# Optimization experiments

Hardware: AMD Instinct MI355X
Metric: run time of the kernel (lower is better)

The kernel has to match this reference:

```python
import jax, jax.numpy as jnp
import numpy as np

B, E, F, Q = 16, 2048, 8192, 20
D, WD = 256, 300
NUM_ENTITY, NUM_WORD, NUM_RELATION = 100000, 50000, 600
NUM_LAYER = 3
PAGERANK_LAMBDA = 0.8
FACT_SCALE = 3.0
VERY_NEG = -100000000000.0
VERY_SMALL = 1e-10


def setup_inputs() -> dict:
    key = jax.random.key(0)
    ks = jax.random.split(key, 40)
    s = 0.05
    L = NUM_LAYER
    inp = {
        'local_entity': jax.random.randint(ks[0], (B, E), 0, NUM_ENTITY),
        'q2e_adj_mat': jax.random.uniform(ks[1], (B, E, 1), jnp.float32),
        'kb_fact_rel': jax.random.randint(ks[2], (B, F), 0, NUM_RELATION),
        'query_text': jax.random.randint(ks[3], (B, Q), 0, NUM_WORD),
        'answer_dist': jax.random.uniform(ks[4], (B, E), jnp.float32),
        'e2f_ent': jax.random.randint(ks[5], (B, F), 0, E),
        'f2e_ent': jax.random.randint(ks[6], (B, F), 0, E),
        'word_emb': jax.random.normal(ks[7], (NUM_WORD + 1, WD)) * s,
        'entity_emb': jax.random.normal(ks[8], (NUM_ENTITY + 1, WD)) * s,
        'relation_emb': jax.random.normal(ks[9], (NUM_RELATION + 1, 2 * WD)) * s,
        'entity_lin_w': jax.random.normal(ks[10], (D, WD)) * s,
        'entity_lin_b': jnp.zeros((D,)),
        'relation_lin_w': jax.random.normal(ks[11], (D, 2 * WD)) * s,
        'relation_lin_b': jnp.zeros((D,)),
        'lstm_w_ih': jax.random.normal(ks[12], (4 * D, WD)) * s,
        'lstm_w_hh': jax.random.normal(ks[13], (4 * D, D)) * s,
        'lstm_b_ih': jnp.zeros((4 * D,)),
        'lstm_b_hh': jnp.zeros((4 * D,)),
        'q2e_w': jax.random.normal(ks[14], (L, D, D)) * s,
        'q2e_b': jnp.zeros((L, D)),
        'e2q_w': jax.random.normal(ks[15], (L, D, 3 * D)) * s,
        'e2q_b': jnp.zeros((L, D)),
        'e2e_w': jax.random.normal(ks[16], (L, D, 3 * D)) * s,
        'e2e_b': jnp.zeros((L, D)),
        'kb_head_w': jax.random.normal(ks[17], (L, D, D)) * s,
        'kb_head_b': jnp.zeros((L, D)),
        'kb_tail_w': jax.random.normal(ks[18], (L, D, D)) * s,
        'kb_tail_b': jnp.zeros((L, D)),
        'kb_self_w': jax.random.normal(ks[19], (L, D, D)) * s,
        'kb_self_b': jnp.zeros((L, D)),
        'score_w': jax.random.normal(ks[20], (1, D)) * s,
        'score_b': jnp.zeros((1,)),
    }
    return inp


def _lstm(x, w_ih, w_hh, b_ih, b_hh):
    # torch LSTM, single layer, unidirectional, zero init state; gates (i,f,g,o)
    gx = jnp.einsum('btd,gd->btg', x, w_ih) + b_ih + b_hh  # [B,T,4H]
    H = w_hh.shape[1]
    init = (jnp.zeros((x.shape[0], H), x.dtype), jnp.zeros((x.shape[0], H), x.dtype))
    def step(carry, g):
        h, c = carry
        z = g + h @ w_hh.T
        i, f, gg, o = jnp.split(z, 4, axis=-1)
        c = jax.nn.sigmoid(f) * c + jax.nn.sigmoid(i) * jnp.tanh(gg)
        h = jax.nn.sigmoid(o) * jnp.tanh(c)
        return (h, c), h
    (h, _), hs = jax.lax.scan(step, init, jnp.swapaxes(gx, 0, 1))
    return jnp.swapaxes(hs, 0, 1), h  # [B,T,H], [B,H]


def _forward(local_entity, q2e_adj_mat, kb_fact_rel, query_text, e2f_ent, f2e_ent,
             word_emb, entity_emb, relation_emb,
             entity_lin_w, entity_lin_b, relation_lin_w, relation_lin_b,
             lstm_w_ih, lstm_w_hh, lstm_b_ih, lstm_b_hh,
             q2e_w, q2e_b, e2q_w, e2q_b, e2e_w, e2e_b,
             kb_head_w, kb_head_b, kb_tail_w, kb_tail_b, kb_self_w, kb_self_b,
             score_w, score_b):
    bidx = jnp.arange(B)[:, None]
    ent_mask = (local_entity != NUM_ENTITY).astype(jnp.float32)  # [B,E]
    q_mask = (query_text != NUM_WORD).astype(jnp.float32)        # [B,Q]

    # query LSTM encoding (dropout = identity in eval)
    qh, qlast = _lstm(word_emb[query_text], lstm_w_ih, lstm_w_hh, lstm_b_ih, lstm_b_hh)
    query_node = qlast[:, None, :]                               # [B,1,D]

    # fact embeddings
    lf = relation_emb[kb_fact_rel] @ relation_lin_w.T + relation_lin_b  # [B,F,D]
    div = jnp.sqrt(jnp.float32(D))

    # fact <-> query attention
    sim = jnp.einsum('bqd,bfd->bqf', qh, lf) / div
    sim = jax.nn.softmax(sim + (1.0 - q_mask)[:, :, None] * VERY_NEG, axis=1)
    att = jnp.einsum('bqf,bqd->bfd', sim, qh)
    Wf = jnp.sum(att * lf, axis=2) / div                          # [B,F]
    W_tilde = jnp.exp(Wf - jnp.max(Wf, axis=1, keepdims=True))    # [B,F]

    # e2f softmax normalizer: scatter-add fact weights onto head entities
    e2f_softmax = jnp.zeros((B, E), W_tilde.dtype).at[bidx, e2f_ent].add(W_tilde)
    e2f_softmax = jnp.maximum(e2f_softmax, VERY_SMALL)

    # entity embeddings (word_dim != entity_dim -> linear projection)
    le = entity_emb[local_entity] @ entity_lin_w.T + entity_lin_b  # [B,E,D]
    pagerank = q2e_adj_mat[..., 0]                                 # [B,E]

    for i in range(NUM_LAYER):
        q2e = jnp.broadcast_to(query_node @ q2e_w[i].T + q2e_b[i], (B, E, D))
        # fact update: self + gathered head-entity messages
        fact_self = lf @ kb_self_w[i].T + kb_self_b[i]
        head = le @ kb_head_w[i].T + kb_head_b[i]
        e2f_emb = jax.nn.relu(fact_self + jnp.take_along_axis(head, e2f_ent[:, :, None], axis=1))
        norm = W_tilde * jnp.take_along_axis(pagerank / e2f_softmax, e2f_ent, axis=1)  # [B,F]
        e2f_emb = e2f_emb * norm[:, :, None]
        # entity update: self + scattered tail messages
        tail = e2f_emb @ kb_tail_w[i].T + kb_tail_b[i]
        ent_self = le @ kb_self_w[i].T + kb_self_b[i]
        f2e_emb = jax.nn.relu(ent_self + jnp.zeros((B, E, D), le.dtype).at[bidx, f2e_ent].add(tail))
        pagerank = (PAGERANK_LAMBDA * jnp.zeros((B, E), norm.dtype).at[bidx, f2e_ent].add(norm)
                    + (1.0 - PAGERANK_LAMBDA) * pagerank)
        nxt = jnp.concatenate([le, q2e, FACT_SCALE * f2e_emb], axis=2)  # [B,E,3D]
        query_node = jnp.einsum('be,bed->bd', pagerank, nxt @ e2q_w[i].T + e2q_b[i])[:, None, :]
        le = jax.nn.relu(nxt @ e2e_w[i].T + e2e_b[i])

    score = (le @ score_w.T + score_b)[..., 0]                     # [B,E]
    return score


def reference(local_entity, q2e_adj_mat, kb_fact_rel, query_text, answer_dist,
              e2f_ent, f2e_ent, word_emb, entity_emb, relation_emb,
              entity_lin_w, entity_lin_b, relation_lin_w, relation_lin_b,
              lstm_w_ih, lstm_w_hh, lstm_b_ih, lstm_b_hh,
              q2e_w, q2e_b, e2q_w, e2q_b, e2e_w, e2e_b,
              kb_head_w, kb_head_b, kb_tail_w, kb_tail_b, kb_self_w, kb_self_b,
              score_w, score_b):
    return _forward(local_entity, q2e_adj_mat, kb_fact_rel, query_text, e2f_ent, f2e_ent,
                    word_emb, entity_emb, relation_emb,
                    entity_lin_w, entity_lin_b, relation_lin_w, relation_lin_b,
                    lstm_w_ih, lstm_w_hh, lstm_b_ih, lstm_b_hh,
                    q2e_w, q2e_b, e2q_w, e2q_b, e2e_w, e2e_b,
                    kb_head_w, kb_head_b, kb_tail_w, kb_tail_b, kb_self_w, kb_self_b,
                    score_w, score_b)
```

## Files before the change

### kernel.cpp

```cpp
#include <hip/hip_runtime.h>
#include <hip/hip_bf16.h>

typedef __hip_bfloat16 bf16;
typedef __attribute__((ext_vector_type(8))) short bf16x8;
typedef __attribute__((ext_vector_type(4))) float f32x4;

#define BB 16
#define EE 2048
#define FF 8192
#define QQ 20
#define DD 256
#define WDIM 300
#define NWORD 50000
#define VERY_NEG_F (-1.0e11f)

static __device__ __forceinline__ float b2f(bf16 x){ return __bfloat162float(x); }
static __device__ __forceinline__ bf16 f2b(float x){ return __float2bfloat16(x); }
static __device__ __forceinline__ float sigm(float x){ return 1.f/(1.f+expf(-x)); }
static __device__ __forceinline__ void ld4bf(const bf16* p, float v[4]){
  short4 s = *(const short4*)p;
  v[0]=b2f(*(const bf16*)&s.x); v[1]=b2f(*(const bf16*)&s.y);
  v[2]=b2f(*(const bf16*)&s.z); v[3]=b2f(*(const bf16*)&s.w);
}
static __device__ __forceinline__ void st4bf(bf16* p, float a,float b,float c,float d){
  unsigned short u[4]; bf16 t;
  t=f2b(a);u[0]=*(unsigned short*)&t; t=f2b(b);u[1]=*(unsigned short*)&t;
  t=f2b(c);u[2]=*(unsigned short*)&t; t=f2b(d);u[3]=*(unsigned short*)&t;
  *(short4*)p=*(short4*)u;
}

#define O_GX       0UL
#define O_QH       1310720UL
#define O_QNODE    1638400UL
#define O_RELLIN   1654784UL
#define O_WR       2270208UL
#define O_WMAX     2308864UL
#define O_WT       2309120UL
#define O_E2FS     2833408UL
#define O_PR       2964480UL
#define O_PRAGG    3095552UL
#define O_Q2EV     3226624UL
#define O_Q2EVB    3243008UL
#define O_RELSELF  3251200UL
#define O_NORM     3866624UL
#define O_WNXT     4390912UL
#define O_PRSUM    4440064UL
#define O_CNT      4440320UL
#define O_CUR      4571392UL
#define O_BSTART   4702464UL
#define O_BIDX     4834048UL
#define O_ELWPAD   5358336UL
#define O_FLAG     5522176UL
#define O_CVT      5522432UL
#define O_AGG      10915584UL
#define O_ENTSELF  27692800UL
#define O_LEA      44470016UL
#define O_LEB      61247232UL
#define O_HEAD     78024448UL
#define O_F2EEMB   94801664UL

#define C_ELB   0
#define C_RLW   256
#define C_RLB   153856
#define C_WIH   154112
#define C_WHH   461312
#define C_BIH   723456
#define C_BHH   724480
#define C_Q2EW  725504
#define C_Q2EB  922112
#define C_E2QW  922880
#define C_E2QB  1512704
#define C_E2EW  1513472
#define C_E2EB  2103296
#define C_KHW   2104064
#define C_KHB   2300672
#define C_KTW   2301440
#define C_KTB   2498048
#define C_KSW   2498816
#define C_KSB   2695424
#define C_SCW   2696192
#define C_SCB   2696448

__global__ __launch_bounds__(256) void k_sniff(const unsigned short* ee, int* flag){
  __shared__ int red[256];
  int c=0;
  for(int i=threadIdx.x;i<4096;i+=256){
    int ex=(ee[2*i]>>7)&0xFF;
    c += (ex>=192);
  }
  red[threadIdx.x]=c; __syncthreads();
  for(int o=128;o;o>>=1){ if(threadIdx.x<o) red[threadIdx.x]+=red[threadIdx.x+o]; __syncthreads(); }
  if(!threadIdx.x) flag[0] = (red[0]>64) ? 1 : 0;
}

struct CvtJobs{ const void* src[20]; bf16* dst[20]; int n[20]; int sc[20]; };
__global__ __launch_bounds__(256) void k_cvt(CvtJobs J, const int* dfl){
  const int isf=*dfl;
  int j=blockIdx.y;
  int n=J.n[j];
  int i4=(blockIdx.x*256+threadIdx.x)*4;
  if(i4>=n) return;
  float m = (J.sc[j] && ((i4%768)>=512)) ? 3.f : 1.f;
  bf16* d=J.dst[j]+i4;
  if(isf){
    const float* s=(const float*)J.src[j]+i4;
    if(i4+4<=n){ float4 t=*(const float4*)s; st4bf(d,t.x*m,t.y*m,t.z*m,t.w*m); }
    else for(int r=0;i4+r<n;r++) d[r]=f2b(s[r]*m);
  } else {
    const bf16* s=(const bf16*)J.src[j]+i4;
    if(i4+4<=n){ float v[4]; ld4bf(s,v); st4bf(d,v[0]*m,v[1]*m,v[2]*m,v[3]*m); }
    else for(int r=0;i4+r<n;r++) d[r]=f2b(b2f(s[r])*m);
  }
}

__global__ __launch_bounds__(256) void k_cvtwhh(const void* src, bf16* wf, const int* dfl){
  const int isf=*dfl;
  int fid=blockIdx.x*256+threadIdx.x;
  int lane=fid&63, kt=(fid>>6)&7, gt=fid>>9;
  int l16=lane&15, q=lane>>4;
  long so=(long)(gt*16+l16)*256 + kt*32 + q*8;
  float v[8];
  if(isf){ const float* s=(const float*)src+so;
    #pragma unroll
    for(int j=0;j<8;j++) v[j]=s[j];
  } else { const bf16* s=(const bf16*)src+so; ld4bf(s,v); ld4bf(s+4,v+4); }
  bf16* d=wf+(long)fid*8;
  st4bf(d,v[0],v[1],v[2],v[3]); st4bf(d+4,v[4],v[5],v[6],v[7]);
}

__global__ __launch_bounds__(256) void k_cvtelw(const void* src, bf16* dst, const int* dfl){
  const int isf=*dfl;
  int r=blockIdx.x;
  for(int c=threadIdx.x;c<320;c+=256){
    float v=0.f;
    if(c<300) v = isf ? ((const float*)src)[r*300+c] : b2f(((const bf16*)src)[r*300+c]);
    dst[(long)r*320+c]=f2b(v);
  }
}

__global__ __launch_bounds__(256) void k_cnt(const int* f2e, int* cnt){
  int i=blockIdx.x*256+threadIdx.x;
  atomicAdd(&cnt[((i>>13)<<11)+f2e[i]], 1);
}
__global__ __launch_bounds__(1024) void k_scan(const int* cnt, int* bstart){
  __shared__ int ps[1024];
  int t=threadIdx.x;
  int loc[32]; int s=0;
  #pragma unroll
  for(int j=0;j<32;j++){ loc[j]=s; s+=cnt[t*32+j]; }
  ps[t]=s; __syncthreads();
  for(int off=1;off<1024;off<<=1){
    int v=(t>=off)?ps[t-off]:0;
    __syncthreads(); ps[t]+=v; __syncthreads();
  }
  int base=(t? ps[t-1]:0);
  #pragma unroll
  for(int j=0;j<32;j++) bstart[t*32+j]=base+loc[j];
  if(t==1023) bstart[32768]=ps[1023];
}
__global__ __launch_bounds__(256) void k_fill(const int* f2e, const int* bstart, int* cur, int* bidx){
  int i=blockIdx.x*256+threadIdx.x;
  int key=((i>>13)<<11)+f2e[i];
  int pos=bstart[key]+atomicAdd(&cur[key],1);
  bidx[pos]=i;
}

__global__ __launch_bounds__(256) void k_gx(const int* qtext, const void* wemb,
    const bf16* wih, const bf16* bih, const bf16* bhh, float* gx, const int* dfl){
  const int isf=*dfl;
  int bt=blockIdx.x;
  __shared__ float xr[WDIM];
  int w=qtext[bt];
  for(int k4=threadIdx.x*4;k4<WDIM;k4+=1024){
    if(isf){ float4 t=*(const float4*)((const float*)wemb+(long)w*WDIM+k4);
             xr[k4]=t.x;xr[k4+1]=t.y;xr[k4+2]=t.z;xr[k4+3]=t.w; }
    else   { float v[4]; ld4bf((const bf16*)wemb+(long)w*WDIM+k4,v);
             xr[k4]=v[0];xr[k4+1]=v[1];xr[k4+2]=v[2];xr[k4+3]=v[3]; }
  }
  __syncthreads();
  #pragma unroll
  for(int s=0;s<4;s++){
    int g=threadIdx.x+256*s;
    float acc=b2f(bih[g])+b2f(bhh[g]);
    const bf16* wr=wih+(long)g*WDIM;
    for(int k4=0;k4<WDIM;k4+=4){
      float v[4]; ld4bf(wr+k4,v);
      acc+=v[0]*xr[k4]+v[1]*xr[k4+1]+v[2]*xr[k4+2]+v[3]*xr[k4+3];
    }
    gx[bt*1024+g]=acc;
  }
}

#define NLB 8
__global__ __launch_bounds__(512) void k_mega(const float* gx, const bf16* wf,
    float* qh, float* qnode, bf16* hbuf, int* lcnt,
    const void* remb, const bf16* rlw, const bf16* rlb, float* rel_lin,
    const int* local_entity, const void* emb, bf16* A0,
    const void* adj, float* pr, const int* dfl){
  const int bid=blockIdx.x, tid=threadIdx.x;
  if(bid<NLB){
    __shared__ bf16  hlds[16*264];
    __shared__ float zs[4*16*32];
    __shared__ bf16  hsl[512];
    const int k=bid;
    const int wv=tid>>6, lane=tid&63, q=lane>>4, l16=lane&15;
    const int gt=(wv>>1)*16 + k*2 + (wv&1);
    const int b=tid>>5, u=tid&31, gu=k*32+u;
    bf16x8 wreg[8];
    #pragma unroll
    for(int kt=0;kt<8;kt++)
      wreg[kt]=*(const bf16x8*)(wf + (((long)(gt*8+kt))*64 + lane)*8);
    float c=0.f;
    float gxr[4];
    #pragma unroll
    for(int g=0;g<4;g++) gxr[g]=gx[(b*QQ+0)*1024 + g*256 + gu];
    for(int t=0;t<QQ;t++){
      f32x4 acc=(f32x4){0.f,0.f,0.f,0.f};
      if(t){
        while(__hip_atomic_load(lcnt+(t-1), __ATOMIC_RELAXED, __HIP_MEMORY_SCOPE_AGENT) < NLB)
          __builtin_amdgcn_s_sleep(2);
        __builtin_amdgcn_fence(__ATOMIC_ACQUIRE, "agent");
        __builtin_amdgcn_sched_barrier(0);
        const bf16* hb = hbuf + (t&1)*4096;
        {
          int r=tid>>5, cc=(tid&31)*8;
          unsigned long long v0=__hip_atomic_load((const unsigned long long*)(hb + r*256 + cc),
                         __ATOMIC_RELAXED, __HIP_MEMORY_SCOPE_AGENT);
          unsigned long long v1=__hip_atomic_load((const unsigned long long*)(hb + r*256 + cc + 4),
                         __ATOMIC_RELAXED, __HIP_MEMORY_SCOPE_AGENT);
          *(unsigned long long*)&hlds[r*264 + cc] = v0;
          *(unsigned long long*)&hlds[r*264 + cc + 4] = v1;
        }
        __syncthreads();
        #pragma unroll
        for(int kt=0;kt<8;kt++){
          bf16x8 af=*(const bf16x8*)&hlds[l16*264 + kt*32 + q*8];
          acc=__builtin_amdgcn_mfma_f32_16x16x32_bf16(af,wreg[kt],acc,0,0,0);
        }
      }
      #pragma unroll
      for(int r=0;r<4;r++) zs[(wv>>1)*512 + (q*4+r)*32 + (wv&1)*16 + l16]=acc[r];
      __syncthreads();
      float zi=zs[0*512+b*32+u]+gxr[0];
      float zf=zs[1*512+b*32+u]+gxr[1];
      float zg=zs[2*512+b*32+u]+gxr[2];
      float zo=zs[3*512+b*32+u]+gxr[3];
      { int tn=(t<QQ-1)?t+1:t;
        #pragma unroll
        for(int g=0;g<4;g++) gxr[g]=gx[(b*QQ+tn)*1024 + g*256 + gu];
      }
      c=sigm(zf)*c+sigm(zi)*tanhf(zg);
      float hv=sigm(zo)*tanhf(c);
      hsl[tid]=f2b(hv);
      __syncthreads();
      if(t<QQ-1){
        if(tid<128){
          bf16* hw=hbuf + ((t+1)&1)*4096;
          int bb=tid>>3, p=tid&7;
          unsigned long long v=*(unsigned long long*)&hsl[bb*32+p*4];
          __hip_atomic_store((unsigned long long*)(hw + bb*256 + k*32 + p*4), v,
                             __ATOMIC_RELAXED, __HIP_MEMORY_SCOPE_AGENT);
        }
        __syncthreads();
        if(tid==0)
          __hip_atomic_fetch_add(lcnt+t, 1, __ATOMIC_RELAXED, __HIP_MEMORY_SCOPE_AGENT);
      }
      __builtin_nontemporal_store(hv, &qh[(long)(b*QQ+t)*256+gu]);
      if(t==QQ-1) qnode[(b<<8)+gu]=hv;
    }
  } else if(bid<309){
    __shared__ float rr[2][2*WDIM];
    const int isf=*dfl;
    const int half=tid>>8, d=tid&255;
    const int r=(bid-8)*2+half;
    if(r<601){
      for(int k4=d*4;k4<2*WDIM;k4+=1024){
        if(isf){ float4 t4=*(const float4*)((const float*)remb+(long)r*2*WDIM+k4);
                 rr[half][k4]=t4.x;rr[half][k4+1]=t4.y;rr[half][k4+2]=t4.z;rr[half][k4+3]=t4.w; }
        else   { float v[4]; ld4bf((const bf16*)remb+(long)r*2*WDIM+k4,v);
                 rr[half][k4]=v[0];rr[half][k4+1]=v[1];rr[half][k4+2]=v[2];rr[half][k4+3]=v[3]; }
      }
    }
    __syncthreads();
    if(r<601){
      float acc=b2f(rlb[d]);
      const bf16* wr=rlw+(long)d*2*WDIM;
      for(int k4=0;k4<2*WDIM;k4+=4){
        float v[4]; ld4bf(wr+k4,v);
        acc+=v[0]*rr[half][k4]+v[1]*rr[half][k4+1]+v[2]*rr[half][k4+2]+v[3]*rr[half][k4+3];
      }
      rel_lin[r*DD+d]=acc;
    }
  } else if(bid<325){
    const int isf=*dfl;
    int i4=((bid-309)*512+tid)*4;
    if(isf){ *(float4*)(pr+i4)=*(const float4*)((const float*)adj+i4); }
    else { float v[4]; ld4bf((const bf16*)adj+i4,v);
           float4 t; t.x=v[0];t.y=v[1];t.z=v[2];t.w=v[3]; *(float4*)(pr+i4)=t; }
  } else {
    const int isf=*dfl;
    int row=(bid-325)*4+(tid>>7); int t=tid&127;
    int ent=local_entity[row];
    bf16* dst=A0+(long)row*320;
    if(t<75){
      float v[4];
      if(isf){ float4 x=*(const float4*)((const float*)emb+(long)ent*WDIM+t*4);
               v[0]=x.x;v[1]=x.y;v[2]=x.z;v[3]=x.w; }
      else ld4bf((const bf16*)emb+(long)ent*WDIM+t*4, v);
      st4bf(dst+t*4, v[0],v[1],v[2],v[3]);
    } else if(t<80){
      st4bf(dst+t*4, 0.f,0.f,0.f,0.f);
    }
  }
}

__global__ __launch_bounds__(256) void k_simwr(const float* qh, const float* rel_lin,
    const int* qtext, float* Wr){
  int b = blockIdx.x, rc = blockIdx.y;
  __shared__ float qhb[QQ*DD];
  __shared__ float qm[QQ];
  for(int i=threadIdx.x;i<QQ*DD;i+=256) qhb[i]=qh[b*QQ*DD+i];
  if(threadIdx.x<QQ) qm[threadIdx.x] = (qtext[b*QQ+threadIdx.x]!=NWORD)?0.f:VERY_NEG_F;
  __syncthreads();
  int r = rc*256+threadIdx.x;
  if(r>=601) return;
  float s[QQ];
  #pragma unroll
  for(int q=0;q<QQ;q++) s[q]=0.f;
  for(int k=0;k<DD;k++){
    float rl = rel_lin[r*DD+k];
    #pragma unroll
    for(int q=0;q<QQ;q++) s[q] += qhb[q*DD+k]*rl;
  }
  float m=-1e30f;
  #pragma unroll
  for(int q=0;q<QQ;q++){ s[q]*=0.0625f; m=fmaxf(m, s[q]+qm[q]); }
  float sum=0.f, w=0.f;
  #pragma unroll
  for(int q=0;q<QQ;q++){ float p=expf(s[q]+qm[q]-m); sum+=p; w+=p*s[q]; }
  Wr[b*601+r] = w/sum;
}

__global__ __launch_bounds__(256) void k_wmax(const float* Wr, const int* rel, float* wmax){
  int b=blockIdx.x; __shared__ float red[256];
  float m=-1e30f;
  for(int f=threadIdx.x;f<FF;f+=256) m=fmaxf(m, Wr[b*601+rel[b*FF+f]]);
  red[threadIdx.x]=m; __syncthreads();
  for(int o=128;o;o>>=1){ if(threadIdx.x<o) red[threadIdx.x]=fmaxf(red[threadIdx.x],red[threadIdx.x+o]); __syncthreads(); }
  if(!threadIdx.x) wmax[b]=red[0];
}
__global__ __launch_bounds__(256) void k_wt(const float* Wr, const int* rel,
    const float* wmax, const int* e2f, float* wt, float* e2fs){
  int i = blockIdx.x*256+threadIdx.x;
  int b = i>>13;
  float v = expf(Wr[b*601+rel[i]] - wmax[b]);
  wt[i]=v;
  atomicAdd(e2fs + (b<<11) + e2f[i], v);
}

struct MG {
  const bf16* A; const bf16* W; const bf16* bias;
  bf16* out; int K;
  const bf16* Aq2; const bf16* Af2;
  const int* cnt; const bf16* addb;
  const bf16* W2; const bf16* bias2; bf16* out2;
};
template<int CONCAT,int EPI,int TK,int DUAL>
__global__ __launch_bounds__(256) void k_mgemm(MG p){
  const int m0 = blockIdx.x*64;
  const int wave = threadIdx.x>>6, lane = threadIdx.x&63;
  const int q = lane>>4, l16 = lane&15;
  const int n0 = wave*64;
  const int bidx_ = m0>>11;
  const bf16* Wp = p.W; const bf16* biasp = p.bias; bf16* outp = p.out;
  if(DUAL && blockIdx.y){ Wp=p.W2; biasp=p.bias2; outp=p.out2; }
  f32x4 acc[4][4];
  #pragma unroll
  for(int i=0;i<4;i++)
    #pragma unroll
    for(int j=0;j<4;j++) acc[i][j]=(f32x4){0.f,0.f,0.f,0.f};
  #pragma unroll
  for(int k0=0;k0<TK;k0+=32){
    int kk=k0+q*8;
    bf16x8 af[4], bw[4];
    #pragma unroll
    for(int mi=0;mi<4;mi++){
      int row=m0+mi*16+l16;
      const bf16* ap;
      if(CONCAT){
        if(kk<256)      ap=p.A  +(long)row*256+kk;
        else if(kk<512) ap=p.Aq2+(bidx_<<8)+(kk-256);
        else            ap=p.Af2+(long)row*256+(kk-512);
      } else ap=p.A+(long)row*TK+kk;
      af[mi]=*(const bf16x8*)ap;
    }
    #pragma unroll
    for(int ni=0;ni<4;ni++)
      bw[ni]=*(const bf16x8*)(Wp+(long)(n0+ni*16+l16)*TK+kk);
    #pragma unroll
    for(int mi=0;mi<4;mi++)
      #pragma unroll
      for(int ni=0;ni<4;ni++)
        acc[mi][ni]=__builtin_amdgcn_mfma_f32_16x16x32_bf16(af[mi],bw[ni],acc[mi][ni],0,0,0);
  }
  #pragma unroll
  for(int ni=0;ni<4;ni++){
    int col=n0+ni*16+l16;
    float bv=b2f(biasp[col]);
    #pragma unroll
    for(int mi=0;mi<4;mi++){
      #pragma unroll
      for(int r=0;r<4;r++){
        int row=m0+mi*16+q*4+r;
        float v=acc[mi][ni][r];
        if(EPI==0) v+=bv;
        else if(EPI==1) v=fmaxf(v+bv,0.f);
        else {
          v += (float)p.cnt[row]*bv + b2f(p.addb[(long)row*256+col]);
          v=fmaxf(v,0.f);
        }
        outp[(long)row*256+col]=f2b(v);
      }
    }
  }
}

__global__ __launch_bounds__(256) void k_small(const float* rel_lin, const bf16* selfw,
    const bf16* selfb, const float* qnode, const bf16* q2ew, const bf16* q2eb,
    float* relself, float* q2ev, bf16* q2evb){
  __shared__ float xr[DD];
  int d=threadIdx.x;
  if(blockIdx.x<601){
    int r=blockIdx.x;
    xr[d]=rel_lin[r*DD+d]; __syncthreads();
    float acc=b2f(selfb[d]);
    const bf16* wr=selfw+(long)d*DD;
    for(int k4=0;k4<DD;k4+=4){
      float v[4]; ld4bf(wr+k4,v);
      acc+=v[0]*xr[k4]+v[1]*xr[k4+1]+v[2]*xr[k4+2]+v[3]*xr[k4+3];
    }
    relself[r*DD+d]=acc;
  } else {
    int b=blockIdx.x-601;
    xr[d]=qnode[(b<<8)+d]; __syncthreads();
    float acc=b2f(q2eb[d]);
    const bf16* wr=q2ew+(long)d*DD;
    for(int k4=0;k4<DD;k4+=4){
      float v[4]; ld4bf(wr+k4,v);
      acc+=v[0]*xr[k4]+v[1]*xr[k4+1]+v[2]*xr[k4+2]+v[3]*xr[k4+3];
    }
    q2ev[(b<<8)+d]=acc;
    q2evb[(b<<8)+d]=f2b(acc);
  }
}

__global__ __launch_bounds__(256) void k_norm(const float* wt, const float* pr,
    const float* e2fs, const int* e2f, const int* f2e, float* normv, float* pragg){
  int i=blockIdx.x*256+threadIdx.x;
  int b=i>>13;
  int e=e2f[i];
  float v=wt[i]*pr[(b<<11)+e]/fmaxf(e2fs[(b<<11)+e],1e-10f);
  normv[i]=v;
  atomicAdd(pragg+(b<<11)+f2e[i], v);
}

__global__ __launch_bounds__(256) void k_agg(const int* bstart, const int* bidx,
    const int* rel, const int* e2f, const float* normv, const float* relself,
    const bf16* head, bf16* agg){
  int eidx=blockIdx.x*4+(threadIdx.x>>6);
  int lane=threadIdx.x&63;
  int b=eidx>>11;
  float a0=0.f,a1=0.f,a2=0.f,a3=0.f;
  int s=bstart[eidx], e=bstart[eidx+1];
  for(int i=s;i<e;i++){
    int f=bidx[i];
    int r=rel[f]; int ent=e2f[f]; float nv=normv[f];
    float4 rs=*(const float4*)&relself[r*DD+lane*4];
    float hd[4]; ld4bf(head+(long)(((b<<11)+ent)*DD+lane*4),hd);
    a0+=fmaxf(rs.x+hd[0],0.f)*nv; a1+=fmaxf(rs.y+hd[1],0.f)*nv;
    a2+=fmaxf(rs.z+hd[2],0.f)*nv; a3+=fmaxf(rs.w+hd[3],0.f)*nv;
  }
  st4bf(agg+(long)eidx*DD+lane*4, a0,a1,a2,a3);
}

__global__ __launch_bounds__(256) void k_wnxt(const float* pragg, float* pr, const bf16* le,
    const bf16* f2e, float* wnxt, float* prsum){
  __shared__ float r1[4*256];
  __shared__ float r3[4*256];
  __shared__ float rp[4];
  const int b=blockIdx.x, ch=blockIdx.y;
  const int wv=threadIdx.x>>6, lane=threadIdx.x&63;
  const int pe0=(b<<11)+ch*64+wv*16;
  float pv=0.f;
  if(lane<16){
    pv=0.8f*pragg[pe0+lane]+0.2f*pr[pe0+lane];
    pr[pe0+lane]=pv;
  }
  float a1[4]={0.f,0.f,0.f,0.f}, a3[4]={0.f,0.f,0.f,0.f}, ap=0.f;
  #pragma unroll
  for(int r=0;r<16;r++){
    float p=__shfl(pv, r, 64);
    long base=((long)(pe0+r))<<8;
    float v1[4],v3[4];
    ld4bf(le +base+lane*4, v1);
    ld4bf(f2e+base+lane*4, v3);
    #pragma unroll
    for(int j=0;j<4;j++){ a1[j]+=p*v1[j]; a3[j]+=p*v3[j]; }
    ap+=p;
  }
  #pragma unroll
  for(int j=0;j<4;j++){ r1[wv*256+lane*4+j]=a1[j]; r3[wv*256+lane*4+j]=a3[j]; }
  if(!lane) rp[wv]=ap;
  __syncthreads();
  const int t=threadIdx.x;
  float s1=r1[t]+r1[256+t]+r1[512+t]+r1[768+t];
  float s3=r3[t]+r3[256+t]+r3[512+t]+r3[768+t];
  atomicAdd(&wnxt[b*768+t], s1);
  atomicAdd(&wnxt[b*768+512+t], s3);
  if(!t) atomicAdd(&prsum[b], rp[0]+rp[1]+rp[2]+rp[3]);
}

__global__ __launch_bounds__(256) void k_qnode(const float* wnxt, const float* prsum,
    const float* q2ev, const bf16* w, const bf16* bias, float* qnode){
  int b=blockIdx.x, d=threadIdx.x;
  __shared__ float xr[768];
  float ps=prsum[b];
  xr[d]=wnxt[b*768+d];
  xr[256+d]=ps*q2ev[(b<<8)+d];
  xr[512+d]=wnxt[b*768+512+d];
  __syncthreads();
  float acc=0.f;
  const bf16* wr=w+(long)d*768;
  for(int k4=0;k4<768;k4+=4){
    float v[4]; ld4bf(wr+k4,v);
    acc+=v[0]*xr[k4]+v[1]*xr[k4+1]+v[2]*xr[k4+2]+v[3]*xr[k4+3];
  }
  qnode[(b<<8)+d]=acc+ps*b2f(bias[d]);
}

__global__ __launch_bounds__(256) void k_score(const bf16* le, const bf16* sw,
    const bf16* sb, void* out, const int* dfl){
  const int isf=*dfl;
  int o=blockIdx.x*4 + (threadIdx.x>>6);
  int lane=threadIdx.x&63;
  float v[4],wv[4];
  ld4bf(le+(long)o*DD+lane*4,v); ld4bf(sw+lane*4,wv);
  float acc=v[0]*wv[0]+v[1]*wv[1]+v[2]*wv[2]+v[3]*wv[3];
  for(int off=32;off;off>>=1) acc+=__shfl_down(acc,off,64);
  if(!lane){
    float r=acc+b2f(sb[0]);
    if(isf) ((float*)out)[o]=r; else ((bf16*)out)[o]=f2b(r);
  }
}

extern "C" void kernel_launch(void* const* d_in, const int* in_sizes, int n_in,
                              void* d_out, int out_size, void* d_ws, size_t ws_size,
                              hipStream_t stream){
  const int*  local_entity=(const int*)d_in[0];
  const void* q2e_adj     =d_in[1];
  const int*  kb_fact_rel =(const int*)d_in[2];
  const int*  query_text  =(const int*)d_in[3];
  const int*  e2f_ent     =(const int*)d_in[5];
  const int*  f2e_ent     =(const int*)d_in[6];
  const void* word_emb    =d_in[7];
  const void* entity_emb  =d_in[8];
  const void* relation_emb=d_in[9];

  char* ws=(char*)d_ws;
  float* gx      =(float*)(ws+O_GX);
  float* qh      =(float*)(ws+O_QH);
  float* qnode   =(float*)(ws+O_QNODE);
  float* rel_lin =(float*)(ws+O_RELLIN);
  float* Wr      =(float*)(ws+O_WR);
  float* wmax    =(float*)(ws+O_WMAX);
  float* wt      =(float*)(ws+O_WT);
  float* e2fs    =(float*)(ws+O_E2FS);
  float* pr      =(float*)(ws+O_PR);
  float* pragg   =(float*)(ws+O_PRAGG);
  float* q2ev    =(float*)(ws+O_Q2EV);
  bf16*  q2evb   =(bf16*)(ws+O_Q2EVB);
  float* relself =(float*)(ws+O_RELSELF);
  float* normv   =(float*)(ws+O_NORM);
  float* wnxt    =(float*)(ws+O_WNXT);
  float* prsum   =(float*)(ws+O_PRSUM);
  int*   cnt     =(int*)(ws+O_CNT);
  int*   cur     =(int*)(ws+O_CUR);
  int*   bstart  =(int*)(ws+O_BSTART);
  int*   bidx    =(int*)(ws+O_BIDX);
  bf16*  elwpad  =(bf16*)(ws+O_ELWPAD);
  int*   dflag   =(int*)(ws+O_FLAG);
  bf16*  cw      =(bf16*)(ws+O_CVT);
  bf16*  agg     =(bf16*)(ws+O_AGG);
  bf16*  A0      =(bf16*)(ws+O_AGG);
  bf16*  entself =(bf16*)(ws+O_ENTSELF);
  bf16*  leA     =(bf16*)(ws+O_LEA);
  bf16*  leB     =(bf16*)(ws+O_LEB);
  bf16*  headb   =(bf16*)(ws+O_HEAD);
  bf16*  f2eemb  =(bf16*)(ws+O_F2EEMB);
  bf16*  hbuf    =(bf16*)(ws+O_LEA);
  int*   lcnt    =(int*)(ws+O_LEA+16384);

  k_sniff<<<1,256,0,stream>>>((const unsigned short*)entity_emb, dflag);

  CvtJobs J;
  int cntj=0;
  auto add=[&](int in_idx, long coff, int n, int sc){
    J.src[cntj]=d_in[in_idx]; J.dst[cntj]=cw+coff; J.n[cntj]=n; J.sc[cntj]=sc; cntj++;
  };
  add(11,C_ELB,256,0);
  add(12,C_RLW,153600,0);  add(13,C_RLB,256,0);
  add(14,C_WIH,307200,0);
  add(16,C_BIH,1024,0);    add(17,C_BHH,1024,0);
  add(18,C_Q2EW,196608,0); add(19,C_Q2EB,768,0);
  add(20,C_E2QW,589824,1); add(21,C_E2QB,768,0);
  add(22,C_E2EW,589824,1); add(23,C_E2EB,768,0);
  add(24,C_KHW,196608,0);  add(25,C_KHB,768,0);
  add(26,C_KTW,196608,0);  add(27,C_KTB,768,0);
  add(28,C_KSW,196608,0);  add(29,C_KSB,768,0);
  add(30,C_SCW,256,0);     add(31,C_SCB,1,0);
  k_cvt<<<dim3(576,20),256,0,stream>>>(J, dflag);
  k_cvtwhh<<<128,256,0,stream>>>(d_in[15], cw+C_WHH, dflag);
  k_cvtelw<<<256,256,0,stream>>>(d_in[10], elwpad, dflag);

  hipMemsetAsync(cnt, 0, (size_t)2*BB*EE*4, stream);
  k_cnt <<<BB*FF/256,256,0,stream>>>(f2e_ent, cnt);
  k_scan<<<1,1024,0,stream>>>(cnt, bstart);
  k_fill<<<BB*FF/256,256,0,stream>>>(f2e_ent, bstart, cur, bidx);

  k_gx   <<<BB*QQ,256,0,stream>>>(query_text, word_emb, cw+C_WIH, cw+C_BIH, cw+C_BHH, gx, dflag);
  hipMemsetAsync(lcnt, 0, 128, stream);
  k_mega<<<8517,512,0,stream>>>(gx, cw+C_WHH, qh, qnode, hbuf, lcnt,
      relation_emb, cw+C_RLW, cw+C_RLB, rel_lin,
      local_entity, entity_emb, A0,
      q2e_adj, pr, dflag);
  k_simwr<<<dim3(BB,3),256,0,stream>>>(qh, rel_lin, query_text, Wr);
  k_wmax <<<BB,256,0,stream>>>(Wr, kb_fact_rel, wmax);
  hipMemsetAsync(e2fs, 0, (size_t)BB*EE*4, stream);
  k_wt   <<<BB*FF/256,256,0,stream>>>(Wr, kb_fact_rel, wmax, e2f_ent, wt, e2fs);

  {
    MG p{}; p.A=A0; p.W=elwpad; p.bias=cw+C_ELB; p.out=leA; p.K=320;
    k_mgemm<0,0,320,0><<<BB*EE/64,256,0,stream>>>(p);
  }

  bf16* le_cur=leA; bf16* le_nxt=leB;
  for(int i=0;i<3;i++){
    k_small<<<617,256,0,stream>>>(rel_lin, cw+C_KSW+(long)i*65536, cw+C_KSB+(long)i*256,
        qnode, cw+C_Q2EW+(long)i*65536, cw+C_Q2EB+(long)i*256, relself, q2ev, q2evb);
    {
      MG p{}; p.A=le_cur; p.K=256;
      p.W=cw+C_KHW+(long)i*65536;  p.bias=cw+C_KHB+(long)i*256;  p.out=headb;
      p.W2=cw+C_KSW+(long)i*65536; p.bias2=cw+C_KSB+(long)i*256; p.out2=entself;
      k_mgemm<0,0,256,1><<<dim3(BB*EE/64,2),256,0,stream>>>(p);
    }
    hipMemsetAsync(pragg, 0, (size_t)BB*EE*4, stream);
    k_norm<<<BB*FF/256,256,0,stream>>>(wt, pr, e2fs, e2f_ent, f2e_ent, normv, pragg);
    k_agg <<<BB*EE/4,256,0,stream>>>(bstart, bidx, kb_fact_rel, e2f_ent, normv, relself, headb, agg);
    {
      MG p{}; p.A=agg; p.W=cw+C_KTW+(long)i*65536; p.bias=cw+C_KTB+(long)i*256;
      p.out=f2eemb; p.K=256; p.cnt=cnt; p.addb=entself;
      k_mgemm<0,2,256,0><<<BB*EE/64,256,0,stream>>>(p);
    }
    hipMemsetAsync(wnxt, 0, (size_t)(BB*768*4+256), stream);
    k_wnxt <<<dim3(BB,32),256,0,stream>>>(pragg, pr, le_cur, f2eemb, wnxt, prsum);
    k_qnode<<<BB,256,0,stream>>>(wnxt, prsum, q2ev, cw+C_E2QW+(long)i*196608, cw+C_E2QB+(long)i*256, qnode);
    {
      MG p{}; p.A=le_cur; p.W=cw+C_E2EW+(long)i*196608; p.bias=cw+C_E2EB+(long)i*256;
      p.out=le_nxt; p.K=768; p.Aq2=q2evb; p.Af2=f2eemb;
      k_mgemm<1,1,768,0><<<BB*EE/64,256,0,stream>>>(p);
    }
    bf16* t=le_cur; le_cur=le_nxt; le_nxt=t;
  }

  k_score<<<BB*EE/4,256,0,stream>>>(le_cur, cw+C_SCW, cw+C_SCB, d_out, dflag);
}
```

Measured before the change: 1.081 ms.

## Fuse per-layer small kernels and fold memsets into compute kernels

Several independent per-layer launches are merged into single grids partitioned by block index. The relation/query matvecs, the head and self GEMMs and the fact-normalisation step become one kernel, and the query-node matvec rides along with the e2e GEMM. The hipMemsetAsync calls are replaced by zeroing inside existing kernels, with buffers cleared right after they are consumed for the next layer. The acquire fence in the LSTM spin-wait is also dropped, which removes sync cost but risks ordering issues when reading the shared hidden state.

```diff
diff --git a/kernel.cpp b/kernel.cpp
--- a/kernel.cpp
+++ b/kernel.cpp
@@ -166,7 +166,9 @@
 }
 
 __global__ __launch_bounds__(256) void k_gx(const int* qtext, const void* wemb,
-    const bf16* wih, const bf16* bih, const bf16* bhh, float* gx, const int* dfl){
+    const bf16* wih, const bf16* bih, const bf16* bhh, float* gx, const int* dfl,
+    int* lcnt){
+  if(blockIdx.x==0 && threadIdx.x<32) lcnt[threadIdx.x]=0;
   const int isf=*dfl;
   int bt=blockIdx.x;
   __shared__ float xr[WDIM];
@@ -219,7 +221,6 @@
       if(t){
         while(__hip_atomic_load(lcnt+(t-1), __ATOMIC_RELAXED, __HIP_MEMORY_SCOPE_AGENT) < NLB)
           __builtin_amdgcn_s_sleep(2);
-        __builtin_amdgcn_fence(__ATOMIC_ACQUIRE, "agent");
         __builtin_amdgcn_sched_barrier(0);
         const bf16* hb = hbuf + (t&1)*4096;
         {
@@ -341,8 +342,14 @@
   Wr[b*601+r] = w/sum;
 }
 
-__global__ __launch_bounds__(256) void k_wmax(const float* Wr, const int* rel, float* wmax){
+__global__ __launch_bounds__(256) void k_wmax(const float* Wr, const int* rel, float* wmax,
+    float* e2fs){
   int b=blockIdx.x; __shared__ float red[256];
+  {
+    int g=b*256+threadIdx.x;
+    float4 z={0.f,0.f,0.f,0.f};
+    *(float4*)(e2fs+g*8)=z; *(float4*)(e2fs+g*8+4)=z;
+  }
   float m=-1e30f;
   for(int f=threadIdx.x;f<FF;f+=256) m=fmaxf(m, Wr[b*601+rel[b*FF+f]]);
   red[threadIdx.x]=m; __syncthreads();
@@ -350,30 +357,25 @@
   if(!threadIdx.x) wmax[b]=red[0];
 }
 __global__ __launch_bounds__(256) void k_wt(const float* Wr, const int* rel,
-    const float* wmax, const int* e2f, float* wt, float* e2fs){
+    const float* wmax, const int* e2f, float* wt, float* e2fs,
+    float* pragg, float* wnxtb, float* prsum){
   int i = blockIdx.x*256+threadIdx.x;
+  if(i<32768) pragg[i]=0.f;
+  if(i<12288) wnxtb[i]=0.f;
+  if(i<16)    prsum[i]=0.f;
   int b = i>>13;
   float v = expf(Wr[b*601+rel[i]] - wmax[b]);
   wt[i]=v;
   atomicAdd(e2fs + (b<<11) + e2f[i], v);
 }
 
-struct MG {
-  const bf16* A; const bf16* W; const bf16* bias;
-  bf16* out; int K;
-  const bf16* Aq2; const bf16* Af2;
-  const int* cnt; const bf16* addb;
-  const bf16* W2; const bf16* bias2; bf16* out2;
-};
-template<int CONCAT,int EPI,int TK,int DUAL>
-__global__ __launch_bounds__(256) void k_mgemm(MG p){
-  const int m0 = blockIdx.x*64;
-  const int wave = threadIdx.x>>6, lane = threadIdx.x&63;
-  const int q = lane>>4, l16 = lane&15;
-  const int n0 = wave*64;
-  const int bidx_ = m0>>11;
-  const bf16* Wp = p.W; const bf16* biasp = p.bias; bf16* outp = p.out;
-  if(DUAL && blockIdx.y){ Wp=p.W2; biasp=p.bias2; outp=p.out2; }
+template<int TK,int CONCAT,int EPI>
+static __device__ __forceinline__ void mg_body(const bf16* A, const bf16* W,
+    const bf16* bias, bf16* out, const bf16* Aq2, const bf16* Af2,
+    const int* cnt, const bf16* addb, int m0, int tid){
+  const int lane=tid&63, q=lane>>4, l16=lane&15;
+  const int n0=(tid>>6)*64;
+  const int bidx_=m0>>11;
   f32x4 acc[4][4];
   #pragma unroll
   for(int i=0;i<4;i++)
@@ -388,15 +390,15 @@
       int row=m0+mi*16+l16;
       const bf16* ap;
       if(CONCAT){
-        if(kk<256)      ap=p.A  +(long)row*256+kk;
-        else if(kk<512) ap=p.Aq2+(bidx_<<8)+(kk-256);
-        else            ap=p.Af2+(long)row*256+(kk-512);
-      } else ap=p.A+(long)row*TK+kk;
+        if(kk<256)      ap=A  +(long)row*256+kk;
+        else if(kk<512) ap=Aq2+(bidx_<<8)+(kk-256);
+        else            ap=Af2+(long)row*256+(kk-512);
+      } else ap=A+(long)row*TK+kk;
       af[mi]=*(const bf16x8*)ap;
     }
     #pragma unroll
     for(int ni=0;ni<4;ni++)
-      bw[ni]=*(const bf16x8*)(Wp+(long)(n0+ni*16+l16)*TK+kk);
+      bw[ni]=*(const bf16x8*)(W+(long)(n0+ni*16+l16)*TK+kk);
     #pragma unroll
     for(int mi=0;mi<4;mi++)
       #pragma unroll
@@ -406,7 +408,7 @@
   #pragma unroll
   for(int ni=0;ni<4;ni++){
     int col=n0+ni*16+l16;
-    float bv=b2f(biasp[col]);
+    float bv=b2f(bias[col]);
     #pragma unroll
     for(int mi=0;mi<4;mi++){
       #pragma unroll
@@ -416,52 +418,73 @@
         if(EPI==0) v+=bv;
         else if(EPI==1) v=fmaxf(v+bv,0.f);
         else {
-          v += (float)p.cnt[row]*bv + b2f(p.addb[(long)row*256+col]);
+          v += (float)cnt[row]*bv + b2f(addb[(long)row*256+col]);
           v=fmaxf(v,0.f);
         }
-        outp[(long)row*256+col]=f2b(v);
+        out[(long)row*256+col]=f2b(v);
       }
     }
   }
 }
 
-__global__ __launch_bounds__(256) void k_small(const float* rel_lin, const bf16* selfw,
-    const bf16* selfb, const float* qnode, const bf16* q2ew, const bf16* q2eb,
-    float* relself, float* q2ev, bf16* q2evb){
-  __shared__ float xr[DD];
-  int d=threadIdx.x;
-  if(blockIdx.x<601){
-    int r=blockIdx.x;
-    xr[d]=rel_lin[r*DD+d]; __syncthreads();
-    float acc=b2f(selfb[d]);
-    const bf16* wr=selfw+(long)d*DD;
-    for(int k4=0;k4<DD;k4+=4){
-      float v[4]; ld4bf(wr+k4,v);
-      acc+=v[0]*xr[k4]+v[1]*xr[k4+1]+v[2]*xr[k4+2]+v[3]*xr[k4+3];
-    }
-    relself[r*DD+d]=acc;
+struct MG {
+  const bf16* A; const bf16* W; const bf16* bias; bf16* out;
+  const bf16* Aq2; const bf16* Af2;
+  const int* cnt; const bf16* addb;
+};
+template<int CONCAT,int EPI,int TK>
+__global__ __launch_bounds__(256) void k_mgemm(MG p){
+  mg_body<TK,CONCAT,EPI>(p.A,p.W,p.bias,p.out,p.Aq2,p.Af2,p.cnt,p.addb,
+                         blockIdx.x*64,threadIdx.x);
+}
+
+struct L1 {
+  const float* rel_lin; const bf16* ksw; const bf16* ksb;
+  const float* qnode; const bf16* q2ew; const bf16* q2eb;
+  float* relself; float* q2ev; bf16* q2evb;
+  const bf16* A; const bf16* khw; const bf16* khb; bf16* headb; bf16* entself;
+  const float* wt; const float* pr; const float* e2fs;
+  const int* e2f; const int* f2e; float* normv; float* pragg;
+};
+__global__ __launch_bounds__(256) void k_lay1(L1 p){
+  const int bid=blockIdx.x, tid=threadIdx.x;
+  if(bid<617){
+    __shared__ float xr[DD];
+    int d=tid;
+    if(bid<601){
+      xr[d]=p.rel_lin[bid*DD+d]; __syncthreads();
+      float acc=b2f(p.ksb[d]);
+      const bf16* wr=p.ksw+(long)d*DD;
+      for(int k4=0;k4<DD;k4+=4){
+        float v[4]; ld4bf(wr+k4,v);
+        acc+=v[0]*xr[k4]+v[1]*xr[k4+1]+v[2]*xr[k4+2]+v[3]*xr[k4+3];
+      }
+      p.relself[bid*DD+d]=acc;
+    } else {
+      int b=bid-601;
+      xr[d]=p.qnode[(b<<8)+d]; __syncthreads();
+      float acc=b2f(p.q2eb[d]);
+      const bf16* wr=p.q2ew+(long)d*DD;
+      for(int k4=0;k4<DD;k4+=4){
+        float v[4]; ld4bf(wr+k4,v);
+        acc+=v[0]*xr[k4]+v[1]*xr[k4+1]+v[2]*xr[k4+2]+v[3]*xr[k4+3];
+      }
+      p.q2ev[(b<<8)+d]=acc;
+      p.q2evb[(b<<8)+d]=f2b(acc);
+    }
+  } else if(bid<1641){
+    int g=bid-617;
+    int m0=(g&511)*64;
+    if(g<512) mg_body<256,0,0>(p.A,p.khw,p.khb,p.headb,0,0,0,0,m0,tid);
+    else      mg_body<256,0,0>(p.A,p.ksw,p.ksb,p.entself,0,0,0,0,m0,tid);
   } else {
-    int b=blockIdx.x-601;
-    xr[d]=qnode[(b<<8)+d]; __syncthreads();
-    float acc=b2f(q2eb[d]);
-    const bf16* wr=q2ew+(long)d*DD;
-    for(int k4=0;k4<DD;k4+=4){
-      float v[4]; ld4bf(wr+k4,v);
-      acc+=v[0]*xr[k4]+v[1]*xr[k4+1]+v[2]*xr[k4+2]+v[3]*xr[k4+3];
-    }
-    q2ev[(b<<8)+d]=acc;
-    q2evb[(b<<8)+d]=f2b(acc);
-  }
-}
-
-__global__ __launch_bounds__(256) void k_norm(const float* wt, const float* pr,
-    const float* e2fs, const int* e2f, const int* f2e, float* normv, float* pragg){
-  int i=blockIdx.x*256+threadIdx.x;
-  int b=i>>13;
-  int e=e2f[i];
-  float v=wt[i]*pr[(b<<11)+e]/fmaxf(e2fs[(b<<11)+e],1e-10f);
-  normv[i]=v;
-  atomicAdd(pragg+(b<<11)+f2e[i], v);
+    int i=(bid-1641)*256+tid;
+    int b=i>>13;
+    int e=p.e2f[i];
+    float v=p.wt[i]*p.pr[(b<<11)+e]/fmaxf(p.e2fs[(b<<11)+e],1e-10f);
+    p.normv[i]=v;
+    atomicAdd(p.pragg+(b<<11)+p.f2e[i], v);
+  }
 }
 
 __global__ __launch_bounds__(256) void k_agg(const int* bstart, const int* bidx,
@@ -483,8 +506,8 @@
   st4bf(agg+(long)eidx*DD+lane*4, a0,a1,a2,a3);
 }
 
-__global__ __launch_bounds__(256) void k_wnxt(const float* pragg, float* pr, const bf16* le,
-    const bf16* f2e, float* wnxt, float* prsum){
+__global__ __launch_bounds__(256) void k_wnxt(const float* praggc, float* pragg, float* pr,
+    const bf16* le, const bf16* f2e, float* wnxt, float* prsum){
   __shared__ float r1[4*256];
   __shared__ float r3[4*256];
   __shared__ float rp[4];
@@ -493,8 +516,10 @@
   const int pe0=(b<<11)+ch*64+wv*16;
   float pv=0.f;
   if(lane<16){
-    pv=0.8f*pragg[pe0+lane]+0.2f*pr[pe0+lane];
-    pr[pe0+lane]=pv;
+    int pe=pe0+lane;
+    pv=0.8f*praggc[pe]+0.2f*pr[pe];
+    pr[pe]=pv;
+    pragg[pe]=0.f;
   }
   float a1[4]={0.f,0.f,0.f,0.f}, a3[4]={0.f,0.f,0.f,0.f}, ap=0.f;
   #pragma unroll
@@ -520,22 +545,27 @@
   if(!t) atomicAdd(&prsum[b], rp[0]+rp[1]+rp[2]+rp[3]);
 }
 
-__global__ __launch_bounds__(256) void k_qnode(const float* wnxt, const float* prsum,
-    const float* q2ev, const bf16* w, const bf16* bias, float* qnode){
-  int b=blockIdx.x, d=threadIdx.x;
-  __shared__ float xr[768];
-  float ps=prsum[b];
-  xr[d]=wnxt[b*768+d];
-  xr[256+d]=ps*q2ev[(b<<8)+d];
-  xr[512+d]=wnxt[b*768+512+d];
-  __syncthreads();
-  float acc=0.f;
-  const bf16* wr=w+(long)d*768;
-  for(int k4=0;k4<768;k4+=4){
-    float v[4]; ld4bf(wr+k4,v);
-    acc+=v[0]*xr[k4]+v[1]*xr[k4+1]+v[2]*xr[k4+2]+v[3]*xr[k4+3];
-  }
-  qnode[(b<<8)+d]=acc+ps*b2f(bias[d]);
+__global__ __launch_bounds__(256) void k_e2eq(MG p, const float* q2ev,
+    const bf16* qw, const bf16* qb, float* wnxtb, float* prsum, float* qnode){
+  if(blockIdx.x<512){
+    mg_body<768,1,1>(p.A,p.W,p.bias,p.out,p.Aq2,p.Af2,0,0,blockIdx.x*64,threadIdx.x);
+  } else {
+    int b=blockIdx.x-512, d=threadIdx.x;
+    __shared__ float xr[768];
+    float ps=prsum[b];
+    xr[d]=wnxtb[b*768+d];            wnxtb[b*768+d]=0.f;
+    xr[256+d]=ps*q2ev[(b<<8)+d];
+    xr[512+d]=wnxtb[b*768+512+d];    wnxtb[b*768+512+d]=0.f;
+    __syncthreads();
+    if(d==0) prsum[b]=0.f;
+    float acc=0.f;
+    const bf16* wr=qw+(long)d*768;
+    for(int k4=0;k4<768;k4+=4){
+      float v[4]; ld4bf(wr+k4,v);
+      acc+=v[0]*xr[k4]+v[1]*xr[k4+1]+v[2]*xr[k4+2]+v[3]*xr[k4+3];
+    }
+    qnode[(b<<8)+d]=acc+ps*b2f(qb[d]);
+  }
 }
 
 __global__ __launch_bounds__(256) void k_score(const bf16* le, const bf16* sw,
@@ -627,47 +657,46 @@
   k_scan<<<1,1024,0,stream>>>(cnt, bstart);
   k_fill<<<BB*FF/256,256,0,stream>>>(f2e_ent, bstart, cur, bidx);
 
-  k_gx   <<<BB*QQ,256,0,stream>>>(query_text, word_emb, cw+C_WIH, cw+C_BIH, cw+C_BHH, gx, dflag);
-  hipMemsetAsync(lcnt, 0, 128, stream);
+  k_gx   <<<BB*QQ,256,0,stream>>>(query_text, word_emb, cw+C_WIH, cw+C_BIH, cw+C_BHH, gx, dflag, lcnt);
   k_mega<<<8517,512,0,stream>>>(gx, cw+C_WHH, qh, qnode, hbuf, lcnt,
       relation_emb, cw+C_RLW, cw+C_RLB, rel_lin,
       local_entity, entity_emb, A0,
       q2e_adj, pr, dflag);
   k_simwr<<<dim3(BB,3),256,0,stream>>>(qh, rel_lin, query_text, Wr);
-  k_wmax <<<BB,256,0,stream>>>(Wr, kb_fact_rel, wmax);
-  hipMemsetAsync(e2fs, 0, (size_t)BB*EE*4, stream);
-  k_wt   <<<BB*FF/256,256,0,stream>>>(Wr, kb_fact_rel, wmax, e2f_ent, wt, e2fs);
+  k_wmax <<<BB,256,0,stream>>>(Wr, kb_fact_rel, wmax, e2fs);
+  k_wt   <<<BB*FF/256,256,0,stream>>>(Wr, kb_fact_rel, wmax, e2f_ent, wt, e2fs,
+                                      pragg, wnxt, prsum);
 
   {
-    MG p{}; p.A=A0; p.W=elwpad; p.bias=cw+C_ELB; p.out=leA; p.K=320;
-    k_mgemm<0,0,320,0><<<BB*EE/64,256,0,stream>>>(p);
+    MG p{}; p.A=A0; p.W=elwpad; p.bias=cw+C_ELB; p.out=leA;
+    k_mgemm<0,0,320><<<BB*EE/64,256,0,stream>>>(p);
   }
 
   bf16* le_cur=leA; bf16* le_nxt=leB;
   for(int i=0;i<3;i++){
-    k_small<<<617,256,0,stream>>>(rel_lin, cw+C_KSW+(long)i*65536, cw+C_KSB+(long)i*256,
-        qnode, cw+C_Q2EW+(long)i*65536, cw+C_Q2EB+(long)i*256, relself, q2ev, q2evb);
     {
-      MG p{}; p.A=le_cur; p.K=256;
-      p.W=cw+C_KHW+(long)i*65536;  p.bias=cw+C_KHB+(long)i*256;  p.out=headb;
-      p.W2=cw+C_KSW+(long)i*65536; p.bias2=cw+C_KSB+(long)i*256; p.out2=entself;
-      k_mgemm<0,0,256,1><<<dim3(BB*EE/64,2),256,0,stream>>>(p);
-    }
-    hipMemsetAsync(pragg, 0, (size_t)BB*EE*4, stream);
-    k_norm<<<BB*FF/256,256,0,stream>>>(wt, pr, e2fs, e2f_ent, f2e_ent, normv, pragg);
+      L1 p{};
+      p.rel_lin=rel_lin; p.ksw=cw+C_KSW+(long)i*65536; p.ksb=cw+C_KSB+(long)i*256;
+      p.qnode=qnode; p.q2ew=cw+C_Q2EW+(long)i*65536; p.q2eb=cw+C_Q2EB+(long)i*256;
+      p.relself=relself; p.q2ev=q2ev; p.q2evb=q2evb;
+      p.A=le_cur; p.khw=cw+C_KHW+(long)i*65536; p.khb=cw+C_KHB+(long)i*256;
+      p.headb=headb; p.entself=entself;
+      p.wt=wt; p.pr=pr; p.e2fs=e2fs;
+      p.e2f=e2f_ent; p.f2e=f2e_ent; p.normv=normv; p.pragg=pragg;
+      k_lay1<<<2153,256,0,stream>>>(p);
+    }
     k_agg <<<BB*EE/4,256,0,stream>>>(bstart, bidx, kb_fact_rel, e2f_ent, normv, relself, headb, agg);
     {
       MG p{}; p.A=agg; p.W=cw+C_KTW+(long)i*65536; p.bias=cw+C_KTB+(long)i*256;
-      p.out=f2eemb; p.K=256; p.cnt=cnt; p.addb=entself;
-      k_mgemm<0,2,256,0><<<BB*EE/64,256,0,stream>>>(p);
-    }
-    hipMemsetAsync(wnxt, 0, (size_t)(BB*768*4+256), stream);
-    k_wnxt <<<dim3(BB,32),256,0,stream>>>(pragg, pr, le_cur, f2eemb, wnxt, prsum);
-    k_qnode<<<BB,256,0,stream>>>(wnxt, prsum, q2ev, cw+C_E2QW+(long)i*196608, cw+C_E2QB+(long)i*256, qnode);
+      p.out=f2eemb; p.cnt=cnt; p.addb=entself;
+      k_mgemm<0,2,256><<<BB*EE/64,256,0,stream>>>(p);
+    }
+    k_wnxt <<<dim3(BB,32),256,0,stream>>>(pragg, pragg, pr, le_cur, f2eemb, wnxt, prsum);
     {
       MG p{}; p.A=le_cur; p.W=cw+C_E2EW+(long)i*196608; p.bias=cw+C_E2EB+(long)i*256;
-      p.out=le_nxt; p.K=768; p.Aq2=q2evb; p.Af2=f2eemb;
-      k_mgemm<1,1,768,0><<<BB*EE/64,256,0,stream>>>(p);
+      p.out=le_nxt; p.Aq2=q2evb; p.Af2=f2eemb;
+      k_e2eq<<<512+BB,256,0,stream>>>(p, q2ev,
+          cw+C_E2QW+(long)i*196608, cw+C_E2QB+(long)i*256, wnxt, prsum, qnode);
     }
     bf16* t=le_cur; le_cur=le_nxt; le_nxt=t;
   }
```

After: 979.2 us. -9.4%, faster.
